# Kernel tuning notes

Hardware: AMD Instinct MI355X
Metric: run time of the kernel (lower is better)

## Reference

```python
import jax, jax.numpy as jnp
import numpy as np
from jax import lax

B, TENC, TMEL = 32, 512, 400
E, H, A, P, M, F, K = 512, 512, 512, 256, 128, 32, 31


def setup_inputs() -> dict:
    key = jax.random.key(0)
    ks = jax.random.split(key, 20)
    def rn(i, shape, fan_in):
        return jax.random.normal(ks[i], shape, jnp.float32) / np.float32(np.sqrt(fan_in))
    return dict(
        enc_outputs=jax.random.normal(ks[0], (B, TENC, 2 * E), jnp.float32),
        mel_spec_true=jax.random.normal(ks[1], (B, TMEL, M), jnp.float32),
        text_lens=jax.random.randint(ks[2], (B,), 0, TENC),
        mel_spec_lens=jax.random.randint(ks[3], (B,), 0, TMEL),
        max_text_len=TENC,
        pre_w1=rn(4, (M, P), M), pre_w2=rn(5, (P, P), P),
        attn_wi=rn(6, (P + E, 3 * H), P + E), attn_wh=rn(7, (H, 3 * H), H),
        attn_bi=jnp.zeros((3 * H,), jnp.float32), attn_bh=jnp.zeros((3 * H,), jnp.float32),
        q_w=rn(8, (H, A), H), k_w=rn(9, (2 * E, A), 2 * E),
        score_w=rn(10, (A, 1), A), score_b=jnp.zeros((1,), jnp.float32),
        loc_conv_w=rn(11, (F, 2, K), 2 * K), loc_w=rn(12, (F, A), F), loc_b=jnp.zeros((A,), jnp.float32),
        out_wi=rn(13, (A + H, 3 * H), A + H), out_wh=rn(14, (H, 3 * H), H),
        out_bi=jnp.zeros((3 * H,), jnp.float32), out_bh=jnp.zeros((3 * H,), jnp.float32),
        dec_w=rn(15, (H + A, M), H + A), dec_b=jnp.zeros((M,), jnp.float32),
        gate_w=rn(16, (H + A, 1), H + A), gate_b=jnp.zeros((1,), jnp.float32),
    )


def _gru_step(x, h, wi, wh, bi, bh):
    # single-step torch nn.GRU cell; gate order r, z, n
    gi = x @ wi + bi
    gh = h @ wh + bh
    ir, iz, inn = jnp.split(gi, 3, axis=-1)
    hr, hz, hn = jnp.split(gh, 3, axis=-1)
    r = jax.nn.sigmoid(ir + hr)
    z = jax.nn.sigmoid(iz + hz)
    n = jnp.tanh(inn + r * hn)
    return (1.0 - z) * n + z * h


def reference(enc_outputs, mel_spec_true, text_lens, mel_spec_lens, max_text_len,
              pre_w1, pre_w2, attn_wi, attn_wh, attn_bi, attn_bh,
              q_w, k_w, score_w, score_b, loc_conv_w, loc_w, loc_b,
              out_wi, out_wh, out_bi, out_bh, dec_w, dec_b, gate_w, gate_b):
    Bsz, Tenc, _ = enc_outputs.shape
    Tmel = mel_spec_true.shape[1]
    Hd = attn_wh.shape[0]
    Ad = k_w.shape[1]
    pad = (loc_conv_w.shape[2] - 1) // 2

    keys_p = enc_outputs @ k_w                                # [B,Tenc,A]
    enc_mask = jnp.arange(Tenc)[None, :] > text_lens[:, None]  # True = masked (t > len)

    def prenet(x):  # dropout disabled for determinism
        return jax.nn.relu(jax.nn.relu(x @ pre_w1) @ pre_w2)

    dec_in0 = prenet(jnp.zeros((Bsz, mel_spec_true.shape[2]), enc_outputs.dtype))
    carry0 = (jnp.zeros((Bsz, Hd), jnp.float32), jnp.zeros((Bsz, Hd), jnp.float32),
              jnp.zeros((Bsz, Tenc), jnp.float32), jnp.zeros((Bsz, Tenc), jnp.float32),
              jnp.zeros((Bsz, Ad), jnp.float32), dec_in0)

    def step(carry, _):
        h_attn, h_out, att_w, att_cum, ctx, dec_in = carry
        h_attn = _gru_step(jnp.concatenate([dec_in, ctx], -1), h_attn, attn_wi, attn_wh, attn_bi, attn_bh)
        loc_in = jnp.stack([att_w, att_cum], axis=1)           # [B,2,Tenc]
        loc = lax.conv_general_dilated(loc_in, loc_conv_w, (1,), [(pad, pad)],
                                       dimension_numbers=('NCH', 'OIH', 'NCH'))  # [B,F,Tenc]
        loc = jnp.swapaxes(loc, 1, 2) @ loc_w + loc_b          # [B,Tenc,A]
        q = (h_attn @ q_w)[:, None, :]                         # [B,1,A]
        s = (jnp.tanh(q + keys_p + loc) @ score_w + score_b)[..., 0]  # [B,Tenc]
        s = jnp.where(enc_mask, -jnp.inf, s)
        att_w = jax.nn.softmax(s, axis=1)
        ctx = jnp.einsum('bt,bta->ba', att_w, keys_p)
        att_cum = att_cum + att_w
        h_out = _gru_step(jnp.concatenate([h_attn, ctx], -1), h_out, out_wi, out_wh, out_bi, out_bh)
        att_h = jnp.concatenate([h_out, ctx], -1)
        mel = att_h @ dec_w + dec_b                            # [B,M]
        stop = (att_h @ gate_w + gate_b)[:, 0]                 # [B]
        dec_in = prenet(mel)                                   # teacher_force_ratio = 0
        return (h_attn, h_out, att_w, att_cum, ctx, dec_in), (mel, stop, att_w)

    _, (mels, gates, attns) = lax.scan(step, carry0, None, length=Tmel)
    mels = jnp.swapaxes(mels, 0, 1)    # [B,Tmel,M]
    gates = jnp.swapaxes(gates, 0, 1)  # [B,Tmel]
    attns = jnp.swapaxes(attns, 0, 1)  # [B,Tmel,Tenc]
    mel_mask = jnp.arange(Tmel)[None, :] > mel_spec_lens[:, None]
    masked_mel = jnp.where(mel_mask[:, :, None], 0.0, mels)
    masked_gate = jnp.where(mel_mask, 1000.0, gates)
    return masked_mel, masked_gate, attns, mel_mask
```

## Files before the change

kernel.cpp:

```cpp
#include <hip/hip_runtime.h>
#include <hip/hip_fp16.h>
#include <math.h>

#define NBLK 256
#define NTHR 1024

__device__ __forceinline__ float fast_rcp(float x) {
#if __has_builtin(__builtin_amdgcn_rcpf)
  return __builtin_amdgcn_rcpf(x);
#else
  return 1.f / x;
#endif
}
__device__ __forceinline__ float fast_sigmoid(float x) { return fast_rcp(1.f + __expf(-x)); }
__device__ __forceinline__ float fast_tanh(float x) { return 1.f - 2.f * fast_rcp(1.f + __expf(2.f * x)); }

union HU2 { unsigned int u; __half2 h; };
union HU4 { uint4 u; __half2 h[4]; };
__device__ __forceinline__ float2 cvt2(unsigned int u) { HU2 t; t.u = u; return __half22float2(t.h); }

__device__ __forceinline__ void sta(float* p, float v) {
  __hip_atomic_store(p, v, __ATOMIC_RELAXED, __HIP_MEMORY_SCOPE_AGENT);
}
__device__ __forceinline__ float lda(const float* p) {
  return __hip_atomic_load(p, __ATOMIC_RELAXED, __HIP_MEMORY_SCOPE_AGENT);
}

struct Params {
  const float *enc, *pre_w1, *pre_w2, *attn_bi, *attn_bh;
  const float *q_w, *k_w, *score_w, *score_b, *conv_w, *loc_w, *loc_b;
  const float *out_bi, *out_bh, *dec_b, *gate_b;
  const float *attn_wi, *attn_wh, *out_wi, *out_wh, *dec_w, *gate_w;
  const int *text_lens, *mel_lens;
  __half *hkeys, *gw1T, *gw2T, *decT, *pre1T, *pre2T, *gateh, *locwh, *qwT;
  float *hA, *hO, *attw, *attcum, *decin, *ebuf, *zpart, *ctxacc, *stateZ;
  int *done;
  unsigned *barc;
  float *out_mel, *out_gate, *out_attn, *out_mask;
};

__device__ __forceinline__ void gbar(unsigned* flags, unsigned* gen, unsigned e,
                                     int blk, int tid) {
  __syncthreads();
  if (tid == 0) {
    asm volatile("s_waitcnt vmcnt(0) lgkmcnt(0)" ::: "memory");
    __hip_atomic_store(&flags[blk], e, __ATOMIC_RELAXED, __HIP_MEMORY_SCOPE_AGENT);
  }
  if (blk == 0) {
    if (tid < 64) {
      while (true) {
        bool ok = true;
#pragma unroll
        for (int j = 0; j < 4; j++) {
          unsigned v = __hip_atomic_load(&flags[tid * 4 + j], __ATOMIC_RELAXED,
                                         __HIP_MEMORY_SCOPE_AGENT);
          ok &= (v >= e);
        }
        if (__all(ok)) break;
        __builtin_amdgcn_s_sleep(1);
      }
      if (tid == 0)
        __hip_atomic_store(gen, e, __ATOMIC_RELAXED, __HIP_MEMORY_SCOPE_AGENT);
    }
  } else {
    if (tid == 0) {
      while (__hip_atomic_load(gen, __ATOMIC_RELAXED, __HIP_MEMORY_SCOPE_AGENT) < e)
        __builtin_amdgcn_s_sleep(2);
    }
  }
  asm volatile("" ::: "memory");
  __syncthreads();
}

__global__ __launch_bounds__(512) void k_keys(Params p) {
  __shared__ float sA[16][132];
  __shared__ float sB[16][68];
  int tid = threadIdx.x;
  int row0 = blockIdx.x * 128, col0 = blockIdx.y * 64;
  float acc[4][4] = {};
  int r = tid >> 2, kq = tid & 3;
  int tx = tid & 15, ty = tid >> 4;
  for (int k0 = 0; k0 < 1024; k0 += 16) {
    __syncthreads();
    float4 a4 = *(const float4*)(p.enc + (size_t)(row0 + r) * 1024 + k0 + kq * 4);
    sA[kq * 4 + 0][r] = a4.x; sA[kq * 4 + 1][r] = a4.y;
    sA[kq * 4 + 2][r] = a4.z; sA[kq * 4 + 3][r] = a4.w;
    if (tid < 256) {
      int kb = tid >> 4, nb = (tid & 15) * 4;
      float4 b4 = *(const float4*)(p.k_w + (size_t)(k0 + kb) * 512 + col0 + nb);
      sB[kb][nb + 0] = b4.x; sB[kb][nb + 1] = b4.y;
      sB[kb][nb + 2] = b4.z; sB[kb][nb + 3] = b4.w;
    }
    __syncthreads();
#pragma unroll
    for (int k = 0; k < 16; k++) {
      float ar[4], br[4];
#pragma unroll
      for (int i = 0; i < 4; i++) { ar[i] = sA[k][ty * 4 + i]; br[i] = sB[k][tx * 4 + i]; }
#pragma unroll
      for (int i = 0; i < 4; i++)
#pragma unroll
        for (int j = 0; j < 4; j++) acc[i][j] = fmaf(ar[i], br[j], acc[i][j]);
    }
  }
#pragma unroll
  for (int i = 0; i < 4; i++)
#pragma unroll
    for (int j = 0; j < 4; j++)
      p.hkeys[(size_t)(row0 + ty * 4 + i) * 512 + col0 + tx * 4 + j] = __float2half(acc[i][j]);
}

__global__ __launch_bounds__(256) void k_repack(Params p) {
  const int gsz = gridDim.x * 256;
  const int t0 = blockIdx.x * 256 + threadIdx.x;
  for (int i = t0; i < 1280 * 512; i += gsz) {
    int r = i >> 9, u = i & 511;
    const float* src = (r < 768) ? p.attn_wi + (size_t)r * 1536 : p.attn_wh + (size_t)(r - 768) * 1536;
    __half2* d = (__half2*)(p.gw1T + ((size_t)i << 2));
    d[0] = __halves2half2(__float2half(src[u]), __float2half(src[512 + u]));
    d[1] = __halves2half2(__float2half(src[1024 + u]), __float2half(0.f));
  }
  for (int i = t0; i < 1536 * 512; i += gsz) {
    int r = i >> 9, u = i & 511;
    const float* src = (r < 1024) ? p.out_wi + (size_t)r * 1536 : p.out_wh + (size_t)(r - 1024) * 1536;
    __half2* d = (__half2*)(p.gw2T + ((size_t)i << 2));
    d[0] = __halves2half2(__float2half(src[u]), __float2half(src[512 + u]));
    d[1] = __halves2half2(__float2half(src[1024 + u]), __float2half(0.f));
  }
  for (int i = t0; i < 512 * 512; i += gsz) {
    int k = i >> 9, a = i & 511;
    p.qwT[(size_t)a * 512 + k] = __float2half(p.q_w[(size_t)k * 512 + a]);
  }
  for (int i = t0; i < 1024 * 128; i += gsz) {
    int k = i >> 7, m = i & 127;
    p.decT[(size_t)m * 1024 + k] = __float2half(p.dec_w[(size_t)k * 128 + m]);
  }
  for (int i = t0; i < 1024; i += gsz) p.gateh[i] = __float2half(p.gate_w[i]);
  for (int i = t0; i < 16384; i += gsz) p.locwh[i] = __float2half(p.loc_w[i]);
  for (int i = t0; i < 128 * 256; i += gsz) {
    int m = i >> 8, pc = i & 255;
    p.pre1T[(size_t)pc * 128 + m] = __float2half(p.pre_w1[(size_t)m * 256 + pc]);
  }
  for (int i = t0; i < 256 * 256; i += gsz) {
    int k = i >> 8, pc = i & 255;
    p.pre2T[(size_t)pc * 256 + k] = __float2half(p.pre_w2[(size_t)k * 256 + pc]);
  }
  for (int i = t0; i < 106496; i += gsz) p.stateZ[i] = 0.f;
  for (int i = t0; i < 16384; i += gsz) p.ctxacc[i] = 0.f;
  for (int i = t0; i < 512; i += gsz) p.barc[i] = 0u;
  for (int i = t0; i < 32; i += gsz) p.done[i] = 0;
  for (int i = t0; i < 12800; i += gsz) {
    int b = i / 400, t = i - b * 400;
    p.out_mask[i] = (t > p.mel_lens[b]) ? 1.f : 0.f;
  }
}

struct SMemMega {
  __half keysL[64 * 512];
  float ctxL[4][512];
  float invZ[4];
  union {
    struct { float x[4][1536]; float4 part4[16][64]; } gr;
    struct { float locS[64][33]; float aw[94]; float ac[94]; float hA_s[512]; float qS[512];
             float qpart[2][512]; float cpred[8][512]; float eS[64]; } s3;
    struct { float xh[1024]; float red[1024]; float mel[128]; float p1[256]; } s6;
  } u;
};

template <int DXI, int RPK>
__device__ __forceinline__ void gru_compute(SMemMega& sm, const uint2* w512,
    const float* __restrict__ bi, const float* __restrict__ bh,
    float* __restrict__ hnext, int ug, int b0, int tid) {
  const int u = tid & 15, b2 = (tid >> 4) & 3, ks = tid >> 6;
  const int uG = (ug << 4) + u;
  float ar = 0.f, az = 0.f, ani = 0.f, anh = 0.f;
  const uint2* w = w512 + (size_t)(ks * RPK) * 512 + uG;
#pragma unroll 8
  for (int j = 0; j < RPK; j++) {
    uint2 wv = w[(size_t)j * 512];
    int r = ks * RPK + j;
    float x = sm.u.gr.x[b2][r];
    float2 f0 = cvt2(wv.x);
    float2 f1 = cvt2(wv.y);
    ar = fmaf(x, f0.x, ar);
    az = fmaf(x, f0.y, az);
    float t = x * f1.x;
    if (r < DXI) ani += t; else anh += t;
  }
  sm.u.gr.part4[ks][(u << 2) + b2] = make_float4(ar, az, ani, anh);
  __syncthreads();
  if (tid < 64) {
    int uu = tid >> 2, bb2 = tid & 3;
    float4 s = make_float4(0.f, 0.f, 0.f, 0.f);
#pragma unroll
    for (int l = 0; l < 16; l++) {
      float4 v = sm.u.gr.part4[l][(uu << 2) + bb2];
      s.x += v.x; s.y += v.y; s.z += v.z; s.w += v.w;
    }
    int uGf = (ug << 4) + uu;
    float r = fast_sigmoid(s.x + bi[uGf] + bh[uGf]);
    float z = fast_sigmoid(s.y + bi[512 + uGf] + bh[512 + uGf]);
    float n = fast_tanh(s.z + bi[1024 + uGf] + r * (s.w + bh[1024 + uGf]));
    float hv = sm.u.gr.x[bb2][DXI + uGf];
    sta(&hnext[((size_t)(b0 + bb2) << 9) + uGf], (1.f - z) * n + z * hv);
  }
}

__global__ __launch_bounds__(NTHR) void mega(Params p) {
  __shared__ SMemMega sm;
  const int blk = blockIdx.x, tid = threadIdx.x;
  const int ug = blk & 31, bg = blk >> 5, b0 = bg * 4;
  const int bS = blk & 31, t8 = blk >> 5, t0g = t8 << 6;
  unsigned epoch = 0;
  unsigned* flags = p.barc;
  unsigned* gen = p.barc + 384;

  {
    const uint4* src = (const uint4*)(p.hkeys + (((size_t)(bS << 9) + t0g) << 9));
    uint4* dst = (uint4*)sm.keysL;
    for (int i = tid; i < 4096; i += NTHR) dst[i] = src[i];
    for (int i = tid; i < 2048; i += NTHR) sm.ctxL[i >> 9][i & 511] = 0.f;
  }
  __syncthreads();

#pragma clang loop unroll(disable)
  for (int step = 0; step < 400; step++) {
    const int par = step & 1;
    float* hA_prev = p.hA + par * 16384;
    float* hA_next = p.hA + (par ^ 1) * 16384;
    float* hO_prev = p.hO + par * 16384;
    float* hO_next = p.hO + (par ^ 1) * 16384;

    {
      if (ug == 0) {
        for (int i = tid; i < 2048; i += NTHR)
          sta(&p.ctxacc[(b0 << 9) + i], 0.f);
      }
      for (int i = tid; i < 1024; i += NTHR) {
        int b2 = i >> 8, r = i & 255;
        sm.u.gr.x[b2][r] = lda(&p.decin[((b0 + b2) << 8) + r]);
      }
      for (int i = tid; i < 2048; i += NTHR) {
        int b2 = i >> 9, a = i & 511;
        sm.u.gr.x[b2][256 + a] = sm.ctxL[b2][a];
      }
      for (int i = tid; i < 2048; i += NTHR) {
        int b2 = i >> 9, a = i & 511;
        sm.u.gr.x[b2][768 + a] = lda(&hA_prev[((b0 + b2) << 9) + a]);
      }
      __syncthreads();
      gru_compute<768, 80>(sm, (const uint2*)p.gw1T, p.attn_bi, p.attn_bh,
                           hA_next, ug, b0, tid);
    }
    gbar(flags, gen, ++epoch, blk, tid);

    {
      const int tlen = p.text_lens[bS];
      for (int j = tid; j < 94; j += NTHR) {
        int pp = t0g - 15 + j;
        bool ok = (unsigned)pp < 512u;
        sm.u.s3.aw[j] = ok ? lda(&p.attw[(bS << 9) + pp]) : 0.f;
        sm.u.s3.ac[j] = ok ? lda(&p.attcum[(bS << 9) + pp]) : 0.f;
      }
      if (tid < 512) sm.u.s3.hA_s[tid] = lda(&hA_next[(bS << 9) + tid]);
      __syncthreads();
      for (int i = tid; i < 2048; i += NTHR) {
        int tt = i >> 5, f = i & 31;
        const float* w0 = p.conv_w + f * 62;
        float a = 0.f;
#pragma unroll
        for (int k = 0; k < 31; k++)
          a = fmaf(w0[k], sm.u.s3.aw[tt + k], fmaf(w0[31 + k], sm.u.s3.ac[tt + k], a));
        sm.u.s3.locS[tt][f] = a;
      }
      {
        int a = tid & 511, ks = tid >> 9;
        const HU4* qp = (const HU4*)(p.qwT + (size_t)a * 512 + ks * 256);
        float q0 = 0.f, q1 = 0.f;
#pragma unroll 4
        for (int it = 0; it < 32; it++) {
          HU4 raw = qp[it];
          int kb = ks * 256 + it * 8;
#pragma unroll
          for (int h2 = 0; h2 < 4; h2++) {
            float2 w = __half22float2(raw.h[h2]);
            q0 = fmaf(sm.u.s3.hA_s[kb + h2 * 2], w.x, q0);
            q1 = fmaf(sm.u.s3.hA_s[kb + h2 * 2 + 1], w.y, q1);
          }
        }
        sm.u.s3.qpart[ks][a] = q0 + q1;
      }
      __syncthreads();
      if (tid < 512)
        sm.u.s3.qS[tid] = sm.u.s3.qpart[0][tid] + sm.u.s3.qpart[1][tid] + p.loc_b[tid];
      __syncthreads();
      const int lane = tid & 63, wv = tid >> 6;
      float acc[4][8];
      float4 qA = *(const float4*)&sm.u.s3.qS[lane * 8];
      float4 qB = *(const float4*)&sm.u.s3.qS[lane * 8 + 4];
#pragma unroll
      for (int j = 0; j < 4; j++) {
        int tL = wv * 4 + j;
        HU4 raw; raw.u = *(const uint4*)&sm.keysL[tL * 512 + lane * 8];
        float2 k0 = __half22float2(raw.h[0]), k1 = __half22float2(raw.h[1]);
        float2 k2 = __half22float2(raw.h[2]), k3 = __half22float2(raw.h[3]);
        acc[j][0] = qA.x + k0.x; acc[j][1] = qA.y + k0.y;
        acc[j][2] = qA.z + k1.x; acc[j][3] = qA.w + k1.y;
        acc[j][4] = qB.x + k2.x; acc[j][5] = qB.y + k2.y;
        acc[j][6] = qB.z + k3.x; acc[j][7] = qB.w + k3.y;
      }
#pragma unroll 4
      for (int f = 0; f < 32; f++) {
        HU4 rw; rw.u = *(const uint4*)(p.locwh + (size_t)f * 512 + lane * 8);
        float2 w0 = __half22float2(rw.h[0]), w1 = __half22float2(rw.h[1]);
        float2 w2 = __half22float2(rw.h[2]), w3 = __half22float2(rw.h[3]);
#pragma unroll
        for (int j = 0; j < 4; j++) {
          float lf = sm.u.s3.locS[wv * 4 + j][f];
          acc[j][0] = fmaf(lf, w0.x, acc[j][0]); acc[j][1] = fmaf(lf, w0.y, acc[j][1]);
          acc[j][2] = fmaf(lf, w1.x, acc[j][2]); acc[j][3] = fmaf(lf, w1.y, acc[j][3]);
          acc[j][4] = fmaf(lf, w2.x, acc[j][4]); acc[j][5] = fmaf(lf, w2.y, acc[j][5]);
          acc[j][6] = fmaf(lf, w3.x, acc[j][6]); acc[j][7] = fmaf(lf, w3.y, acc[j][7]);
        }
      }
      float4 sA = *(const float4*)(p.score_w + lane * 8);
      float4 sB = *(const float4*)(p.score_w + lane * 8 + 4);
      float sbias = p.score_b[0];
      float e_reg[4];
#pragma unroll
      for (int j = 0; j < 4; j++) {
        float pv = fast_tanh(acc[j][0]) * sA.x + fast_tanh(acc[j][1]) * sA.y +
                   fast_tanh(acc[j][2]) * sA.z + fast_tanh(acc[j][3]) * sA.w +
                   fast_tanh(acc[j][4]) * sB.x + fast_tanh(acc[j][5]) * sB.y +
                   fast_tanh(acc[j][6]) * sB.z + fast_tanh(acc[j][7]) * sB.w;
#pragma unroll
        for (int off = 32; off > 0; off >>= 1) pv += __shfl_xor(pv, off, 64);
        int t = t0g + wv * 4 + j;
        e_reg[j] = (t > tlen) ? 0.f : __expf(pv + sbias);
      }
      if (lane == 0) {
#pragma unroll
        for (int j = 0; j < 4; j++) sm.u.s3.eS[wv * 4 + j] = e_reg[j];
      }
      float cp[8] = {0.f, 0.f, 0.f, 0.f, 0.f, 0.f, 0.f, 0.f};
#pragma unroll
      for (int j = 0; j < 4; j++) {
        int tL = wv * 4 + j;
        HU4 raw; raw.u = *(const uint4*)&sm.keysL[tL * 512 + lane * 8];
        float2 k0 = __half22float2(raw.h[0]), k1 = __half22float2(raw.h[1]);
        float2 k2 = __half22float2(raw.h[2]), k3 = __half22float2(raw.h[3]);
        float e = e_reg[j];
        cp[0] = fmaf(e, k0.x, cp[0]); cp[1] = fmaf(e, k0.y, cp[1]);
        cp[2] = fmaf(e, k1.x, cp[2]); cp[3] = fmaf(e, k1.y, cp[3]);
        cp[4] = fmaf(e, k2.x, cp[4]); cp[5] = fmaf(e, k2.y, cp[5]);
        cp[6] = fmaf(e, k3.x, cp[6]); cp[7] = fmaf(e, k3.y, cp[7]);
      }
      __syncthreads();
      if (wv < 8) {
        float4* r0 = (float4*)&sm.u.s3.cpred[wv][lane * 8];
        r0[0] = make_float4(cp[0], cp[1], cp[2], cp[3]);
        r0[1] = make_float4(cp[4], cp[5], cp[6], cp[7]);
      }
      __syncthreads();
      if (wv >= 8) {
        float* r0 = &sm.u.s3.cpred[wv - 8][lane * 8];
#pragma unroll
        for (int i = 0; i < 8; i++) r0[i] += cp[i];
      }
      __syncthreads();
      if (tid < 512) {
        float s = 0.f;
#pragma unroll
        for (int j = 0; j < 8; j++) s += sm.u.s3.cpred[j][tid];
        atomicAdd(&p.ctxacc[(bS << 9) + tid], s);
      }
      if (tid < 64) {
        float e = sm.u.s3.eS[tid];
        sta(&p.ebuf[(bS << 9) + t0g + tid], e);
        float z = e;
#pragma unroll
        for (int off = 32; off > 0; off >>= 1) z += __shfl_xor(z, off, 64);
        if (tid == 0) sta(&p.zpart[bS * 8 + t8], z);
      }
    }
    gbar(flags, gen, ++epoch, blk, tid);

    {
      if (tid < 4) {
        float Z = 0.f;
#pragma unroll
        for (int j = 0; j < 8; j++) Z += lda(&p.zpart[(b0 + tid) * 8 + j]);
        sm.invZ[tid] = fast_rcp(Z);
      }
      __syncthreads();
      for (int i = tid; i < 2048; i += NTHR) {
        int b2 = i >> 9, a = i & 511;
        sm.ctxL[b2][a] = lda(&p.ctxacc[((b0 + b2) << 9) + a]) * sm.invZ[b2];
      }
      if (ug == 0) {
        for (int i = tid; i < 2048; i += NTHR) {
          int b2 = i >> 9, t = i & 511;
          int bb = b0 + b2;
          float v = lda(&p.ebuf[(bb << 9) + t]) * sm.invZ[b2];
          sta(&p.attw[(bb << 9) + t], v);
          float oc = lda(&p.attcum[(bb << 9) + t]);
          sta(&p.attcum[(bb << 9) + t], oc + v);
          p.out_attn[(size_t)bb * 204800 + (size_t)step * 512 + t] = v;
        }
      }
      __syncthreads();
      for (int i = tid; i < 2048; i += NTHR) {
        int b2 = i >> 9, a = i & 511;
        sm.u.gr.x[b2][a] = lda(&hA_next[((b0 + b2) << 9) + a]);
      }
      for (int i = tid; i < 2048; i += NTHR) {
        int b2 = i >> 9, a = i & 511;
        sm.u.gr.x[b2][512 + a] = sm.ctxL[b2][a];
      }
      for (int i = tid; i < 2048; i += NTHR) {
        int b2 = i >> 9, a = i & 511;
        sm.u.gr.x[b2][1024 + a] = lda(&hO_prev[((b0 + b2) << 9) + a]);
      }
      __syncthreads();
      gru_compute<1024, 96>(sm, (const uint2*)p.gw2T, p.out_bi, p.out_bh,
                            hO_next, ug, b0, tid);
      asm volatile("s_waitcnt vmcnt(0)" ::: "memory");
      __syncthreads();
      if (tid < 4) atomicAdd(&p.done[b0 + tid], 1);
      if (ug < 4) {
        const int bb = b0 + ug;
        if (tid == 0) {
          int target = 32 * (step + 1);
          while (__hip_atomic_load(&p.done[bb], __ATOMIC_RELAXED,
                                   __HIP_MEMORY_SCOPE_AGENT) < target)
            __builtin_amdgcn_s_sleep(2);
        }
        __syncthreads();
        sm.u.s6.xh[tid] = (tid < 512) ? lda(&hO_next[(bb << 9) + tid])
                                      : sm.ctxL[ug][tid - 512];
        __syncthreads();
        bool masked = step > p.mel_lens[bb];
        {
          int m = tid & 127, ks = tid >> 7;
          const HU4* dp = (const HU4*)(p.decT + (size_t)m * 1024 + ks * 128);
          float a = 0.f;
#pragma unroll 4
          for (int it = 0; it < 16; it++) {
            HU4 raw = dp[it];
            int kb = ks * 128 + it * 8;
#pragma unroll
            for (int h2 = 0; h2 < 4; h2++) {
              float2 w = __half22float2(raw.h[h2]);
              a = fmaf(sm.u.s6.xh[kb + h2 * 2], w.x, a);
              a = fmaf(sm.u.s6.xh[kb + h2 * 2 + 1], w.y, a);
            }
          }
          sm.u.s6.red[tid] = a;
        }
        __syncthreads();
        if (tid < 128) {
          float mv = p.dec_b[tid];
#pragma unroll
          for (int j = 0; j < 8; j++) mv += sm.u.s6.red[tid + j * 128];
          sm.u.s6.mel[tid] = mv;
          p.out_mel[(size_t)bb * 51200 + (size_t)step * 128 + tid] = masked ? 0.f : mv;
        }
        __syncthreads();
        sm.u.s6.red[tid] = sm.u.s6.xh[tid] * __half2float(p.gateh[tid]);
        __syncthreads();
        if (tid < 64) {
          float g = 0.f;
#pragma unroll
          for (int j = 0; j < 16; j++) g += sm.u.s6.red[tid + j * 64];
#pragma unroll
          for (int off = 32; off > 0; off >>= 1) g += __shfl_xor(g, off, 64);
          if (tid == 0) p.out_gate[bb * 400 + step] = masked ? 1000.f : (g + p.gate_b[0]);
        }
        __syncthreads();
        {
          int pc = tid & 255, ks = tid >> 8;
          const HU4* wp = (const HU4*)(p.pre1T + (size_t)pc * 128 + ks * 32);
          float a = 0.f;
#pragma unroll
          for (int it = 0; it < 4; it++) {
            HU4 raw = wp[it];
            int kb = ks * 32 + it * 8;
#pragma unroll
            for (int h2 = 0; h2 < 4; h2++) {
              float2 w = __half22float2(raw.h[h2]);
              a = fmaf(sm.u.s6.mel[kb + h2 * 2], w.x, a);
              a = fmaf(sm.u.s6.mel[kb + h2 * 2 + 1], w.y, a);
            }
          }
          sm.u.s6.red[tid] = a;
        }
        __syncthreads();
        if (tid < 256) {
          float a = sm.u.s6.red[tid] + sm.u.s6.red[tid + 256] +
                    sm.u.s6.red[tid + 512] + sm.u.s6.red[tid + 768];
          sm.u.s6.p1[tid] = fmaxf(a, 0.f);
        }
        __syncthreads();
        {
          int pc = tid & 255, ks = tid >> 8;
          const HU4* wp = (const HU4*)(p.pre2T + (size_t)pc * 256 + ks * 64);
          float a = 0.f;
#pragma unroll
          for (int it = 0; it < 8; it++) {
            HU4 raw = wp[it];
            int kb = ks * 64 + it * 8;
#pragma unroll
            for (int h2 = 0; h2 < 4; h2++) {
              float2 w = __half22float2(raw.h[h2]);
              a = fmaf(sm.u.s6.p1[kb + h2 * 2], w.x, a);
              a = fmaf(sm.u.s6.p1[kb + h2 * 2 + 1], w.y, a);
            }
          }
          sm.u.s6.red[tid] = a;
        }
        __syncthreads();
        if (tid < 256) {
          float a = sm.u.s6.red[tid] + sm.u.s6.red[tid + 256] +
                    sm.u.s6.red[tid + 512] + sm.u.s6.red[tid + 768];
          sta(&p.decin[(bb << 8) + tid], fmaxf(a, 0.f));
        }
      }
    }
    gbar(flags, gen, ++epoch, blk, tid);
  }
}

extern "C" void kernel_launch(void* const* d_in, const int* in_sizes, int n_in,
                              void* d_out, int out_size, void* d_ws, size_t ws_size,
                              hipStream_t stream) {
  Params p;
  p.enc       = (const float*)d_in[0];
  p.text_lens = (const int*)d_in[2];
  p.mel_lens  = (const int*)d_in[3];
  p.pre_w1    = (const float*)d_in[5];
  p.pre_w2    = (const float*)d_in[6];
  p.attn_wi   = (const float*)d_in[7];
  p.attn_wh   = (const float*)d_in[8];
  p.attn_bi   = (const float*)d_in[9];
  p.attn_bh   = (const float*)d_in[10];
  p.q_w       = (const float*)d_in[11];
  p.k_w       = (const float*)d_in[12];
  p.score_w   = (const float*)d_in[13];
  p.score_b   = (const float*)d_in[14];
  p.conv_w    = (const float*)d_in[15];
  p.loc_w     = (const float*)d_in[16];
  p.loc_b     = (const float*)d_in[17];
  p.out_wi    = (const float*)d_in[18];
  p.out_wh    = (const float*)d_in[19];
  p.out_bi    = (const float*)d_in[20];
  p.out_bh    = (const float*)d_in[21];
  p.dec_w     = (const float*)d_in[22];
  p.dec_b     = (const float*)d_in[23];
  p.gate_w    = (const float*)d_in[24];
  p.gate_b    = (const float*)d_in[25];

  float* ws = (float*)d_ws;
  p.hkeys  = (__half*)(ws);
  p.gw1T   = (__half*)(ws + 4194304);
  p.gw2T   = (__half*)(ws + 5505024);
  p.decT   = (__half*)(ws + 7077888);
  p.pre1T  = (__half*)(ws + 7143424);
  p.pre2T  = (__half*)(ws + 7159808);
  p.gateh  = (__half*)(ws + 7192576);
  p.locwh  = (__half*)(ws + 7193088);
  p.qwT    = (__half*)(ws + 7201280);
  p.hA     = ws + 7332352;
  p.hO     = ws + 7365120;
  p.attw   = ws + 7397888;
  p.attcum = ws + 7414272;
  p.decin  = ws + 7430656;
  p.stateZ = p.hA;
  p.ebuf   = ws + 7438848;
  p.zpart  = ws + 7455232;
  p.ctxacc = ws + 7455488;
  p.done   = (int*)(ws + 7471872);
  p.barc   = (unsigned*)(ws + 7471904);
  float* out = (float*)d_out;
  p.out_mel  = out;
  p.out_gate = out + 1638400;
  p.out_attn = out + 1651200;
  p.out_mask = out + 8204800;

  k_repack<<<2048, 256, 0, stream>>>(p);
  k_keys<<<dim3(128, 8), 512, 0, stream>>>(p);
  void* args[] = { (void*)&p };
  hipLaunchCooperativeKernel((const void*)mega, dim3(NBLK), dim3(NTHR), args, 0, stream);
}
```

Baseline: 41.97 ms.

## Replace global barriers with per-group flag sync and redundantly compute decoder/prenet per block

Removes the three grid-wide centralized barriers per step and replaces them with per-batch-group and per-attention-slice flag arrays, so blocks only wait on the producers they actually depend on. The mel/gate projection and prenet, previously done by only four blocks after an extra counter wait, are now recomputed redundantly in every block at the start of the next step (with an extra trailing step to emit the last outputs). ctxacc is double-buffered by parity so its zeroing does not race with accumulation. This trades extra redundant matvec work and more flag polling for shorter critical-path synchronization.

```diff
diff --git a/kernel.cpp b/kernel.cpp
--- a/kernel.cpp
+++ b/kernel.cpp
@@ -25,51 +25,27 @@
 __device__ __forceinline__ float lda(const float* p) {
   return __hip_atomic_load(p, __ATOMIC_RELAXED, __HIP_MEMORY_SCOPE_AGENT);
 }
+__device__ __forceinline__ int ldai(const int* p) {
+  return __hip_atomic_load(p, __ATOMIC_RELAXED, __HIP_MEMORY_SCOPE_AGENT);
+}
 
 struct Params {
   const float *enc, *pre_w1, *pre_w2, *attn_bi, *attn_bh;
   const float *q_w, *k_w, *score_w, *score_b, *conv_w, *loc_w, *loc_b;
-  const float *out_bi, *out_bh, *dec_b, *gate_b;
-  const float *attn_wi, *attn_wh, *out_wi, *out_wh, *dec_w, *gate_w;
+  const float *out_bi, *out_bh, *dec_b, *gate_b, *gate_w;
+  const float *attn_wi, *attn_wh, *out_wi, *out_wh, *dec_w;
   const int *text_lens, *mel_lens;
-  __half *hkeys, *gw1T, *gw2T, *decT, *pre1T, *pre2T, *gateh, *locwh, *qwT;
-  float *hA, *hO, *attw, *attcum, *decin, *ebuf, *zpart, *ctxacc, *stateZ;
-  int *done;
-  unsigned *barc;
+  __half *hkeys, *gw1T, *gw2T, *decT, *pre1T, *pre2T, *locwh, *qwT;
+  float *hA, *hO, *attw, *attcum, *ebuf, *zpart, *ctxacc, *stateZ;
+  int *flagsA, *flagsB, *flagsC;
   float *out_mel, *out_gate, *out_attn, *out_mask;
 };
 
-__device__ __forceinline__ void gbar(unsigned* flags, unsigned* gen, unsigned e,
-                                     int blk, int tid) {
-  __syncthreads();
+__device__ __forceinline__ void set_flag(int* f, int v, int tid) {
   if (tid == 0) {
     asm volatile("s_waitcnt vmcnt(0) lgkmcnt(0)" ::: "memory");
-    __hip_atomic_store(&flags[blk], e, __ATOMIC_RELAXED, __HIP_MEMORY_SCOPE_AGENT);
-  }
-  if (blk == 0) {
-    if (tid < 64) {
-      while (true) {
-        bool ok = true;
-#pragma unroll
-        for (int j = 0; j < 4; j++) {
-          unsigned v = __hip_atomic_load(&flags[tid * 4 + j], __ATOMIC_RELAXED,
-                                         __HIP_MEMORY_SCOPE_AGENT);
-          ok &= (v >= e);
-        }
-        if (__all(ok)) break;
-        __builtin_amdgcn_s_sleep(1);
-      }
-      if (tid == 0)
-        __hip_atomic_store(gen, e, __ATOMIC_RELAXED, __HIP_MEMORY_SCOPE_AGENT);
-    }
-  } else {
-    if (tid == 0) {
-      while (__hip_atomic_load(gen, __ATOMIC_RELAXED, __HIP_MEMORY_SCOPE_AGENT) < e)
-        __builtin_amdgcn_s_sleep(2);
-    }
-  }
-  asm volatile("" ::: "memory");
-  __syncthreads();
+    __hip_atomic_store(f, v, __ATOMIC_RELAXED, __HIP_MEMORY_SCOPE_AGENT);
+  }
 }
 
 __global__ __launch_bounds__(512) void k_keys(Params p) {
@@ -135,7 +111,6 @@
     int k = i >> 7, m = i & 127;
     p.decT[(size_t)m * 1024 + k] = __float2half(p.dec_w[(size_t)k * 128 + m]);
   }
-  for (int i = t0; i < 1024; i += gsz) p.gateh[i] = __float2half(p.gate_w[i]);
   for (int i = t0; i < 16384; i += gsz) p.locwh[i] = __float2half(p.loc_w[i]);
   for (int i = t0; i < 128 * 256; i += gsz) {
     int m = i >> 8, pc = i & 255;
@@ -145,10 +120,9 @@
     int k = i >> 8, pc = i & 255;
     p.pre2T[(size_t)pc * 256 + k] = __float2half(p.pre_w2[(size_t)k * 256 + pc]);
   }
-  for (int i = t0; i < 106496; i += gsz) p.stateZ[i] = 0.f;
-  for (int i = t0; i < 16384; i += gsz) p.ctxacc[i] = 0.f;
-  for (int i = t0; i < 512; i += gsz) p.barc[i] = 0u;
-  for (int i = t0; i < 32; i += gsz) p.done[i] = 0;
+  for (int i = t0; i < 98304; i += gsz) p.stateZ[i] = 0.f;
+  for (int i = t0; i < 32768; i += gsz) p.ctxacc[i] = 0.f;
+  for (int i = t0; i < 768; i += gsz) p.flagsA[i] = 0;
   for (int i = t0; i < 12800; i += gsz) {
     int b = i / 400, t = i - b * 400;
     p.out_mask[i] = (t > p.mel_lens[b]) ? 1.f : 0.f;
@@ -160,10 +134,10 @@
   float ctxL[4][512];
   float invZ[4];
   union {
-    struct { float x[4][1536]; float4 part4[16][64]; } gr;
+    struct { float x[4][1536]; float4 part4[16][64];
+             float xh[4][1024]; float red[1024]; float mel4[4][128]; float p1b[4][256]; } gr;
     struct { float locS[64][33]; float aw[94]; float ac[94]; float hA_s[512]; float qS[512];
              float qpart[2][512]; float cpred[8][512]; float eS[64]; } s3;
-    struct { float xh[1024]; float red[1024]; float mel[128]; float p1[256]; } s6;
   } u;
 };
 
@@ -211,9 +185,6 @@
   const int blk = blockIdx.x, tid = threadIdx.x;
   const int ug = blk & 31, bg = blk >> 5, b0 = bg * 4;
   const int bS = blk & 31, t8 = blk >> 5, t0g = t8 << 6;
-  unsigned epoch = 0;
-  unsigned* flags = p.barc;
-  unsigned* gen = p.barc + 384;
 
   {
     const uint4* src = (const uint4*)(p.hkeys + (((size_t)(bS << 9) + t0g) << 9));
@@ -224,36 +195,139 @@
   __syncthreads();
 
 #pragma clang loop unroll(disable)
-  for (int step = 0; step < 400; step++) {
+  for (int step = 0; step <= 400; step++) {
     const int par = step & 1;
     float* hA_prev = p.hA + par * 16384;
     float* hA_next = p.hA + (par ^ 1) * 16384;
     float* hO_prev = p.hO + par * 16384;
     float* hO_next = p.hO + (par ^ 1) * 16384;
 
-    {
-      if (ug == 0) {
-        for (int i = tid; i < 2048; i += NTHR)
-          sta(&p.ctxacc[(b0 << 9) + i], 0.f);
-      }
-      for (int i = tid; i < 1024; i += NTHR) {
-        int b2 = i >> 8, r = i & 255;
-        sm.u.gr.x[b2][r] = lda(&p.decin[((b0 + b2) << 8) + r]);
-      }
+    if (tid < 64) {
+      const int* f = p.flagsC + (bg << 5);
+      while (true) {
+        int v = (tid < 32) ? ldai(&f[tid]) : 0x7fffffff;
+        if (__all(v >= step)) break;
+        __builtin_amdgcn_s_sleep(1);
+      }
+    }
+    __syncthreads();
+    if (ug == 0) {
+      for (int i = tid; i < 2048; i += NTHR)
+        sta(&p.ctxacc[((par ^ 1) << 14) + (b0 << 9) + i], 0.f);
+    }
+    for (int i = tid; i < 4096; i += NTHR) {
+      int b2 = i >> 10, r = i & 1023;
+      sm.u.gr.xh[b2][r] = (r < 512) ? lda(&hO_prev[((size_t)(b0 + b2) << 9) + r])
+                                    : sm.ctxL[b2][r - 512];
+    }
+    if (step < 400) {
       for (int i = tid; i < 2048; i += NTHR) {
         int b2 = i >> 9, a = i & 511;
         sm.u.gr.x[b2][256 + a] = sm.ctxL[b2][a];
       }
       for (int i = tid; i < 2048; i += NTHR) {
         int b2 = i >> 9, a = i & 511;
-        sm.u.gr.x[b2][768 + a] = lda(&hA_prev[((b0 + b2) << 9) + a]);
-      }
-      __syncthreads();
-      gru_compute<768, 80>(sm, (const uint2*)p.gw1T, p.attn_bi, p.attn_bh,
-                           hA_next, ug, b0, tid);
-    }
-    gbar(flags, gen, ++epoch, blk, tid);
-
+        sm.u.gr.x[b2][768 + a] = lda(&hA_prev[((size_t)(b0 + b2) << 9) + a]);
+      }
+    }
+    __syncthreads();
+    {
+      int m = tid & 127, b2 = (tid >> 7) & 3, ks = tid >> 9;
+      const HU4* dp = (const HU4*)(p.decT + (size_t)m * 1024 + ks * 512);
+      float a = 0.f;
+#pragma unroll 4
+      for (int it = 0; it < 64; it++) {
+        HU4 raw = dp[it];
+        int kb = ks * 512 + it * 8;
+#pragma unroll
+        for (int h2 = 0; h2 < 4; h2++) {
+          float2 w = __half22float2(raw.h[h2]);
+          a = fmaf(sm.u.gr.xh[b2][kb + h2 * 2], w.x, a);
+          a = fmaf(sm.u.gr.xh[b2][kb + h2 * 2 + 1], w.y, a);
+        }
+      }
+      sm.u.gr.red[tid] = a;
+    }
+    __syncthreads();
+    if (tid < 512) {
+      int m = tid & 127, b2 = tid >> 7;
+      float mv = sm.u.gr.red[tid] + sm.u.gr.red[tid + 512] + p.dec_b[m];
+      sm.u.gr.mel4[b2][m] = mv;
+      if (ug == 0 && step >= 1) {
+        int bb = b0 + b2;
+        bool masked = (step - 1) > p.mel_lens[bb];
+        p.out_mel[(size_t)bb * 51200 + (size_t)(step - 1) * 128 + m] = masked ? 0.f : mv;
+      }
+    }
+    if (ug == 0 && step >= 1 && tid < 256) {
+      int b2 = tid >> 6, lane = tid & 63;
+      float g = 0.f;
+#pragma unroll
+      for (int j = 0; j < 16; j++) {
+        int k = lane + (j << 6);
+        g = fmaf(sm.u.gr.xh[b2][k], p.gate_w[k], g);
+      }
+#pragma unroll
+      for (int off = 32; off > 0; off >>= 1) g += __shfl_xor(g, off, 64);
+      if (lane == 0) {
+        int bb = b0 + b2;
+        bool masked = (step - 1) > p.mel_lens[bb];
+        p.out_gate[bb * 400 + (step - 1)] = masked ? 1000.f : (g + p.gate_b[0]);
+      }
+    }
+    if (step == 400) return;
+    __syncthreads();
+    {
+      int pc = tid & 255, b2 = tid >> 8;
+      const HU4* wp = (const HU4*)(p.pre1T + (size_t)pc * 128);
+      float a = 0.f;
+#pragma unroll 4
+      for (int it = 0; it < 16; it++) {
+        HU4 raw = wp[it];
+        int kb = it * 8;
+#pragma unroll
+        for (int h2 = 0; h2 < 4; h2++) {
+          float2 w = __half22float2(raw.h[h2]);
+          a = fmaf(sm.u.gr.mel4[b2][kb + h2 * 2], w.x, a);
+          a = fmaf(sm.u.gr.mel4[b2][kb + h2 * 2 + 1], w.y, a);
+        }
+      }
+      __syncthreads();
+      sm.u.gr.p1b[b2][pc] = fmaxf(a, 0.f);
+    }
+    __syncthreads();
+    {
+      int pc = tid & 255, b2 = tid >> 8;
+      const HU4* wp = (const HU4*)(p.pre2T + (size_t)pc * 256);
+      float a = 0.f;
+#pragma unroll 4
+      for (int it = 0; it < 32; it++) {
+        HU4 raw = wp[it];
+        int kb = it * 8;
+#pragma unroll
+        for (int h2 = 0; h2 < 4; h2++) {
+          float2 w = __half22float2(raw.h[h2]);
+          a = fmaf(sm.u.gr.p1b[b2][kb + h2 * 2], w.x, a);
+          a = fmaf(sm.u.gr.p1b[b2][kb + h2 * 2 + 1], w.y, a);
+        }
+      }
+      sm.u.gr.x[b2][pc] = (step == 0) ? 0.f : fmaxf(a, 0.f);
+    }
+    __syncthreads();
+    gru_compute<768, 80>(sm, (const uint2*)p.gw1T, p.attn_bi, p.attn_bh,
+                         hA_next, ug, b0, tid);
+    __syncthreads();
+    set_flag(&p.flagsA[blk], step + 1, tid);
+
+    if (tid < 64) {
+      const int* f = p.flagsA + ((bS >> 2) << 5);
+      while (true) {
+        int v = (tid < 32) ? ldai(&f[tid]) : 0x7fffffff;
+        if (__all(v >= step + 1)) break;
+        __builtin_amdgcn_s_sleep(1);
+      }
+    }
+    __syncthreads();
     {
       const int tlen = p.text_lens[bS];
       for (int j = tid; j < 94; j += NTHR) {
@@ -372,7 +446,7 @@
         float s = 0.f;
 #pragma unroll
         for (int j = 0; j < 8; j++) s += sm.u.s3.cpred[j][tid];
-        atomicAdd(&p.ctxacc[(bS << 9) + tid], s);
+        atomicAdd(&p.ctxacc[(par << 14) + (bS << 9) + tid], s);
       }
       if (tid < 64) {
         float e = sm.u.s3.eS[tid];
@@ -383,8 +457,21 @@
         if (tid == 0) sta(&p.zpart[bS * 8 + t8], z);
       }
     }
-    gbar(flags, gen, ++epoch, blk, tid);
-
+    __syncthreads();
+    set_flag(&p.flagsB[blk], step + 1, tid);
+
+    if (tid < 64) {
+      while (true) {
+        int v = 0x7fffffff;
+        if (tid < 32) {
+          int tt8 = tid >> 2, b = b0 + (tid & 3);
+          v = ldai(&p.flagsB[(tt8 << 5) + b]);
+        }
+        if (__all(v >= step + 1)) break;
+        __builtin_amdgcn_s_sleep(1);
+      }
+    }
+    __syncthreads();
     {
       if (tid < 4) {
         float Z = 0.f;
@@ -395,7 +482,7 @@
       __syncthreads();
       for (int i = tid; i < 2048; i += NTHR) {
         int b2 = i >> 9, a = i & 511;
-        sm.ctxL[b2][a] = lda(&p.ctxacc[((b0 + b2) << 9) + a]) * sm.invZ[b2];
+        sm.ctxL[b2][a] = lda(&p.ctxacc[(par << 14) + ((b0 + b2) << 9) + a]) * sm.invZ[b2];
       }
       if (ug == 0) {
         for (int i = tid; i < 2048; i += NTHR) {
@@ -408,125 +495,25 @@
           p.out_attn[(size_t)bb * 204800 + (size_t)step * 512 + t] = v;
         }
       }
-      __syncthreads();
       for (int i = tid; i < 2048; i += NTHR) {
         int b2 = i >> 9, a = i & 511;
-        sm.u.gr.x[b2][a] = lda(&hA_next[((b0 + b2) << 9) + a]);
-      }
+        sm.u.gr.x[b2][a] = lda(&hA_next[((size_t)(b0 + b2) << 9) + a]);
+      }
+      __syncthreads();
       for (int i = tid; i < 2048; i += NTHR) {
         int b2 = i >> 9, a = i & 511;
         sm.u.gr.x[b2][512 + a] = sm.ctxL[b2][a];
       }
       for (int i = tid; i < 2048; i += NTHR) {
         int b2 = i >> 9, a = i & 511;
-        sm.u.gr.x[b2][1024 + a] = lda(&hO_prev[((b0 + b2) << 9) + a]);
+        sm.u.gr.x[b2][1024 + a] = lda(&hO_prev[((size_t)(b0 + b2) << 9) + a]);
       }
       __syncthreads();
       gru_compute<1024, 96>(sm, (const uint2*)p.gw2T, p.out_bi, p.out_bh,
                             hO_next, ug, b0, tid);
-      asm volatile("s_waitcnt vmcnt(0)" ::: "memory");
-      __syncthreads();
-      if (tid < 4) atomicAdd(&p.done[b0 + tid], 1);
-      if (ug < 4) {
-        const int bb = b0 + ug;
-        if (tid == 0) {
-          int target = 32 * (step + 1);
-          while (__hip_atomic_load(&p.done[bb], __ATOMIC_RELAXED,
-                                   __HIP_MEMORY_SCOPE_AGENT) < target)
-            __builtin_amdgcn_s_sleep(2);
-        }
-        __syncthreads();
-        sm.u.s6.xh[tid] = (tid < 512) ? lda(&hO_next[(bb << 9) + tid])
-                                      : sm.ctxL[ug][tid - 512];
-        __syncthreads();
-        bool masked = step > p.mel_lens[bb];
-        {
-          int m = tid & 127, ks = tid >> 7;
-          const HU4* dp = (const HU4*)(p.decT + (size_t)m * 1024 + ks * 128);
-          float a = 0.f;
-#pragma unroll 4
-          for (int it = 0; it < 16; it++) {
-            HU4 raw = dp[it];
-            int kb = ks * 128 + it * 8;
-#pragma unroll
-            for (int h2 = 0; h2 < 4; h2++) {
-              float2 w = __half22float2(raw.h[h2]);
-              a = fmaf(sm.u.s6.xh[kb + h2 * 2], w.x, a);
-              a = fmaf(sm.u.s6.xh[kb + h2 * 2 + 1], w.y, a);
-            }
-          }
-          sm.u.s6.red[tid] = a;
-        }
-        __syncthreads();
-        if (tid < 128) {
-          float mv = p.dec_b[tid];
-#pragma unroll
-          for (int j = 0; j < 8; j++) mv += sm.u.s6.red[tid + j * 128];
-          sm.u.s6.mel[tid] = mv;
-          p.out_mel[(size_t)bb * 51200 + (size_t)step * 128 + tid] = masked ? 0.f : mv;
-        }
-        __syncthreads();
-        sm.u.s6.red[tid] = sm.u.s6.xh[tid] * __half2float(p.gateh[tid]);
-        __syncthreads();
-        if (tid < 64) {
-          float g = 0.f;
-#pragma unroll
-          for (int j = 0; j < 16; j++) g += sm.u.s6.red[tid + j * 64];
-#pragma unroll
-          for (int off = 32; off > 0; off >>= 1) g += __shfl_xor(g, off, 64);
-          if (tid == 0) p.out_gate[bb * 400 + step] = masked ? 1000.f : (g + p.gate_b[0]);
-        }
-        __syncthreads();
-        {
-          int pc = tid & 255, ks = tid >> 8;
-          const HU4* wp = (const HU4*)(p.pre1T + (size_t)pc * 128 + ks * 32);
-          float a = 0.f;
-#pragma unroll
-          for (int it = 0; it < 4; it++) {
-            HU4 raw = wp[it];
-            int kb = ks * 32 + it * 8;
-#pragma unroll
-            for (int h2 = 0; h2 < 4; h2++) {
-              float2 w = __half22float2(raw.h[h2]);
-              a = fmaf(sm.u.s6.mel[kb + h2 * 2], w.x, a);
-              a = fmaf(sm.u.s6.mel[kb + h2 * 2 + 1], w.y, a);
-            }
-          }
-          sm.u.s6.red[tid] = a;
-        }
-        __syncthreads();
-        if (tid < 256) {
-          float a = sm.u.s6.red[tid] + sm.u.s6.red[tid + 256] +
-                    sm.u.s6.red[tid + 512] + sm.u.s6.red[tid + 768];
-          sm.u.s6.p1[tid] = fmaxf(a, 0.f);
-        }
-        __syncthreads();
-        {
-          int pc = tid & 255, ks = tid >> 8;
-          const HU4* wp = (const HU4*)(p.pre2T + (size_t)pc * 256 + ks * 64);
-          float a = 0.f;
-#pragma unroll
-          for (int it = 0; it < 8; it++) {
-            HU4 raw = wp[it];
-            int kb = ks * 64 + it * 8;
-#pragma unroll
-            for (int h2 = 0; h2 < 4; h2++) {
-              float2 w = __half22float2(raw.h[h2]);
-              a = fmaf(sm.u.s6.p1[kb + h2 * 2], w.x, a);
-              a = fmaf(sm.u.s6.p1[kb + h2 * 2 + 1], w.y, a);
-            }
-          }
-          sm.u.s6.red[tid] = a;
-        }
-        __syncthreads();
-        if (tid < 256) {
-          float a = sm.u.s6.red[tid] + sm.u.s6.red[tid + 256] +
-                    sm.u.s6.red[tid + 512] + sm.u.s6.red[tid + 768];
-          sta(&p.decin[(bb << 8) + tid], fmaxf(a, 0.f));
-        }
-      }
-    }
-    gbar(flags, gen, ++epoch, blk, tid);
+    }
+    __syncthreads();
+    set_flag(&p.flagsC[blk], step + 1, tid);
   }
 }
 
@@ -566,20 +553,19 @@
   p.decT   = (__half*)(ws + 7077888);
   p.pre1T  = (__half*)(ws + 7143424);
   p.pre2T  = (__half*)(ws + 7159808);
-  p.gateh  = (__half*)(ws + 7192576);
-  p.locwh  = (__half*)(ws + 7193088);
-  p.qwT    = (__half*)(ws + 7201280);
-  p.hA     = ws + 7332352;
-  p.hO     = ws + 7365120;
-  p.attw   = ws + 7397888;
-  p.attcum = ws + 7414272;
-  p.decin  = ws + 7430656;
+  p.locwh  = (__half*)(ws + 7192576);
+  p.qwT    = (__half*)(ws + 7200768);
+  p.hA     = ws + 7331840;
+  p.hO     = ws + 7364608;
+  p.attw   = ws + 7397376;
+  p.attcum = ws + 7413760;
   p.stateZ = p.hA;
-  p.ebuf   = ws + 7438848;
-  p.zpart  = ws + 7455232;
-  p.ctxacc = ws + 7455488;
-  p.done   = (int*)(ws + 7471872);
-  p.barc   = (unsigned*)(ws + 7471904);
+  p.ebuf   = ws + 7430144;
+  p.zpart  = ws + 7446528;
+  p.ctxacc = ws + 7446784;
+  p.flagsA = (int*)(ws + 7479552);
+  p.flagsB = p.flagsA + 256;
+  p.flagsC = p.flagsA + 512;
   float* out = (float*)d_out;
   p.out_mel  = out;
   p.out_gate = out + 1638400;
```

Result: slower. 61.53 ms (+46.6%).

## Move decoder/prenet stage to next step start and replace grid barrier with targeted flags

Applied to the files above, without the earlier changes.

Moves the mel/gate projection and prenet of step t to the start of step t+1, running on the four blocks per batch group. This lets the tail wait on a per-batch done counter be dropped. The first global barrier after the attention GRU becomes point-to-point flags. Each block waits only for the decin of its own batch group, and the attention-stage block waits only for the 32 GRU blocks that produce its batch. The aim is shorter serialized critical paths and fewer full-grid syncs per step, at the cost of an extra loop iteration and more intricate flag ordering that could race.

```diff
diff --git a/kernel.cpp b/kernel.cpp
--- a/kernel.cpp
+++ b/kernel.cpp
@@ -23,6 +23,9 @@
   __hip_atomic_store(p, v, __ATOMIC_RELAXED, __HIP_MEMORY_SCOPE_AGENT);
 }
 __device__ __forceinline__ float lda(const float* p) {
+  return __hip_atomic_load(p, __ATOMIC_RELAXED, __HIP_MEMORY_SCOPE_AGENT);
+}
+__device__ __forceinline__ int ldai(const int* p) {
   return __hip_atomic_load(p, __ATOMIC_RELAXED, __HIP_MEMORY_SCOPE_AGENT);
 }
 
@@ -34,7 +37,7 @@
   const int *text_lens, *mel_lens;
   __half *hkeys, *gw1T, *gw2T, *decT, *pre1T, *pre2T, *gateh, *locwh, *qwT;
   float *hA, *hO, *attw, *attcum, *decin, *ebuf, *zpart, *ctxacc, *stateZ;
-  int *done;
+  int *flagsA, *flagsD;
   unsigned *barc;
   float *out_mel, *out_gate, *out_attn, *out_mask;
 };
@@ -147,8 +150,8 @@
   }
   for (int i = t0; i < 106496; i += gsz) p.stateZ[i] = 0.f;
   for (int i = t0; i < 16384; i += gsz) p.ctxacc[i] = 0.f;
+  for (int i = t0; i < 288; i += gsz) p.flagsA[i] = 0;
   for (int i = t0; i < 512; i += gsz) p.barc[i] = 0u;
-  for (int i = t0; i < 32; i += gsz) p.done[i] = 0;
   for (int i = t0; i < 12800; i += gsz) {
     int b = i / 400, t = i - b * 400;
     p.out_mask[i] = (t > p.mel_lens[b]) ? 1.f : 0.f;
@@ -224,36 +227,161 @@
   __syncthreads();
 
 #pragma clang loop unroll(disable)
-  for (int step = 0; step < 400; step++) {
+  for (int step = 0; step <= 400; step++) {
     const int par = step & 1;
     float* hA_prev = p.hA + par * 16384;
     float* hA_next = p.hA + (par ^ 1) * 16384;
     float* hO_prev = p.hO + par * 16384;
     float* hO_next = p.hO + (par ^ 1) * 16384;
 
-    {
-      if (ug == 0) {
-        for (int i = tid; i < 2048; i += NTHR)
-          sta(&p.ctxacc[(b0 << 9) + i], 0.f);
-      }
-      for (int i = tid; i < 1024; i += NTHR) {
-        int b2 = i >> 8, r = i & 255;
-        sm.u.gr.x[b2][r] = lda(&p.decin[((b0 + b2) << 8) + r]);
-      }
-      for (int i = tid; i < 2048; i += NTHR) {
-        int b2 = i >> 9, a = i & 511;
-        sm.u.gr.x[b2][256 + a] = sm.ctxL[b2][a];
-      }
-      for (int i = tid; i < 2048; i += NTHR) {
-        int b2 = i >> 9, a = i & 511;
-        sm.u.gr.x[b2][768 + a] = lda(&hA_prev[((b0 + b2) << 9) + a]);
-      }
-      __syncthreads();
-      gru_compute<768, 80>(sm, (const uint2*)p.gw1T, p.attn_bi, p.attn_bh,
-                           hA_next, ug, b0, tid);
-    }
-    gbar(flags, gen, ++epoch, blk, tid);
-
+    if (ug == 0) {
+      for (int i = tid; i < 2048; i += NTHR)
+        sta(&p.ctxacc[(b0 << 9) + i], 0.f);
+    }
+    if (ug < 4) {
+      const int bb = b0 + ug;
+      sm.u.s6.xh[tid] = (tid < 512) ? lda(&hO_prev[(bb << 9) + tid])
+                                    : sm.ctxL[ug][tid - 512];
+      __syncthreads();
+      const int prev = step - 1;
+      bool masked = prev > p.mel_lens[bb];
+      {
+        int m = tid & 127, ks = tid >> 7;
+        const HU4* dp = (const HU4*)(p.decT + (size_t)m * 1024 + ks * 128);
+        float a = 0.f;
+#pragma unroll 4
+        for (int it = 0; it < 16; it++) {
+          HU4 raw = dp[it];
+          int kb = ks * 128 + it * 8;
+#pragma unroll
+          for (int h2 = 0; h2 < 4; h2++) {
+            float2 w = __half22float2(raw.h[h2]);
+            a = fmaf(sm.u.s6.xh[kb + h2 * 2], w.x, a);
+            a = fmaf(sm.u.s6.xh[kb + h2 * 2 + 1], w.y, a);
+          }
+        }
+        sm.u.s6.red[tid] = a;
+      }
+      __syncthreads();
+      if (tid < 128) {
+        float mv = p.dec_b[tid];
+#pragma unroll
+        for (int j = 0; j < 8; j++) mv += sm.u.s6.red[tid + j * 128];
+        sm.u.s6.mel[tid] = mv;
+        if (step >= 1)
+          p.out_mel[(size_t)bb * 51200 + (size_t)prev * 128 + tid] = masked ? 0.f : mv;
+      }
+      __syncthreads();
+      sm.u.s6.red[tid] = sm.u.s6.xh[tid] * __half2float(p.gateh[tid]);
+      __syncthreads();
+      if (tid < 64) {
+        float g = 0.f;
+#pragma unroll
+        for (int j = 0; j < 16; j++) g += sm.u.s6.red[tid + j * 64];
+#pragma unroll
+        for (int off = 32; off > 0; off >>= 1) g += __shfl_xor(g, off, 64);
+        if (tid == 0 && step >= 1)
+          p.out_gate[bb * 400 + prev] = masked ? 1000.f : (g + p.gate_b[0]);
+      }
+      __syncthreads();
+      if (step < 400) {
+        {
+          int pc = tid & 255, ks = tid >> 8;
+          const HU4* wp = (const HU4*)(p.pre1T + (size_t)pc * 128 + ks * 32);
+          float a = 0.f;
+#pragma unroll
+          for (int it = 0; it < 4; it++) {
+            HU4 raw = wp[it];
+            int kb = ks * 32 + it * 8;
+#pragma unroll
+            for (int h2 = 0; h2 < 4; h2++) {
+              float2 w = __half22float2(raw.h[h2]);
+              a = fmaf(sm.u.s6.mel[kb + h2 * 2], w.x, a);
+              a = fmaf(sm.u.s6.mel[kb + h2 * 2 + 1], w.y, a);
+            }
+          }
+          sm.u.s6.red[tid] = a;
+        }
+        __syncthreads();
+        if (tid < 256) {
+          float a = sm.u.s6.red[tid] + sm.u.s6.red[tid + 256] +
+                    sm.u.s6.red[tid + 512] + sm.u.s6.red[tid + 768];
+          sm.u.s6.p1[tid] = fmaxf(a, 0.f);
+        }
+        __syncthreads();
+        {
+          int pc = tid & 255, ks = tid >> 8;
+          const HU4* wp = (const HU4*)(p.pre2T + (size_t)pc * 256 + ks * 64);
+          float a = 0.f;
+#pragma unroll
+          for (int it = 0; it < 8; it++) {
+            HU4 raw = wp[it];
+            int kb = ks * 64 + it * 8;
+#pragma unroll
+            for (int h2 = 0; h2 < 4; h2++) {
+              float2 w = __half22float2(raw.h[h2]);
+              a = fmaf(sm.u.s6.p1[kb + h2 * 2], w.x, a);
+              a = fmaf(sm.u.s6.p1[kb + h2 * 2 + 1], w.y, a);
+            }
+          }
+          sm.u.s6.red[tid] = a;
+        }
+        __syncthreads();
+        if (tid < 256) {
+          float a = sm.u.s6.red[tid] + sm.u.s6.red[tid + 256] +
+                    sm.u.s6.red[tid + 512] + sm.u.s6.red[tid + 768];
+          sta(&p.decin[(bb << 8) + tid], (step == 0) ? 0.f : fmaxf(a, 0.f));
+        }
+        __syncthreads();
+        set_flagD: ;
+        if (tid == 0) {
+          asm volatile("s_waitcnt vmcnt(0) lgkmcnt(0)" ::: "memory");
+          __hip_atomic_store(&p.flagsD[(bg << 2) + ug], step + 1, __ATOMIC_RELAXED,
+                             __HIP_MEMORY_SCOPE_AGENT);
+        }
+      }
+    }
+    if (step == 400) return;
+    __syncthreads();
+    for (int i = tid; i < 2048; i += NTHR) {
+      int b2 = i >> 9, a = i & 511;
+      sm.u.gr.x[b2][256 + a] = sm.ctxL[b2][a];
+    }
+    for (int i = tid; i < 2048; i += NTHR) {
+      int b2 = i >> 9, a = i & 511;
+      sm.u.gr.x[b2][768 + a] = lda(&hA_prev[((size_t)(b0 + b2) << 9) + a]);
+    }
+    if (tid < 64) {
+      while (true) {
+        int v = (tid < 4) ? ldai(&p.flagsD[(bg << 2) + tid]) : 0x7fffffff;
+        if (__all(v >= step + 1)) break;
+        __builtin_amdgcn_s_sleep(1);
+      }
+    }
+    __syncthreads();
+    for (int i = tid; i < 1024; i += NTHR) {
+      int b2 = i >> 8, r = i & 255;
+      sm.u.gr.x[b2][r] = lda(&p.decin[((b0 + b2) << 8) + r]);
+    }
+    __syncthreads();
+    gru_compute<768, 80>(sm, (const uint2*)p.gw1T, p.attn_bi, p.attn_bh,
+                         hA_next, ug, b0, tid);
+    __syncthreads();
+    if (tid == 0) {
+      asm volatile("s_waitcnt vmcnt(0) lgkmcnt(0)" ::: "memory");
+      __hip_atomic_store(&p.flagsA[blk], step + 1, __ATOMIC_RELAXED,
+                         __HIP_MEMORY_SCOPE_AGENT);
+    }
+
+    if (tid < 64) {
+      const int* f = p.flagsA + ((bS >> 2) << 5);
+      while (true) {
+        int v = (tid < 32) ? ldai(&f[tid]) : 0x7fffffff;
+        if (__all(v >= step + 1)) break;
+        __builtin_amdgcn_s_sleep(1);
+      }
+    }
+    __syncthreads();
     {
       const int tlen = p.text_lens[bS];
       for (int j = tid; j < 94; j += NTHR) {
@@ -411,7 +539,7 @@
       __syncthreads();
       for (int i = tid; i < 2048; i += NTHR) {
         int b2 = i >> 9, a = i & 511;
-        sm.u.gr.x[b2][a] = lda(&hA_next[((b0 + b2) << 9) + a]);
+        sm.u.gr.x[b2][a] = lda(&hA_next[((size_t)(b0 + b2) << 9) + a]);
       }
       for (int i = tid; i < 2048; i += NTHR) {
         int b2 = i >> 9, a = i & 511;
@@ -419,112 +547,11 @@
       }
       for (int i = tid; i < 2048; i += NTHR) {
         int b2 = i >> 9, a = i & 511;
-        sm.u.gr.x[b2][1024 + a] = lda(&hO_prev[((b0 + b2) << 9) + a]);
+        sm.u.gr.x[b2][1024 + a] = lda(&hO_prev[((size_t)(b0 + b2) << 9) + a]);
       }
       __syncthreads();
       gru_compute<1024, 96>(sm, (const uint2*)p.gw2T, p.out_bi, p.out_bh,
                             hO_next, ug, b0, tid);
-      asm volatile("s_waitcnt vmcnt(0)" ::: "memory");
-      __syncthreads();
-      if (tid < 4) atomicAdd(&p.done[b0 + tid], 1);
-      if (ug < 4) {
-        const int bb = b0 + ug;
-        if (tid == 0) {
-          int target = 32 * (step + 1);
-          while (__hip_atomic_load(&p.done[bb], __ATOMIC_RELAXED,
-                                   __HIP_MEMORY_SCOPE_AGENT) < target)
-            __builtin_amdgcn_s_sleep(2);
-        }
-        __syncthreads();
-        sm.u.s6.xh[tid] = (tid < 512) ? lda(&hO_next[(bb << 9) + tid])
-                                      : sm.ctxL[ug][tid - 512];
-        __syncthreads();
-        bool masked = step > p.mel_lens[bb];
-        {
-          int m = tid & 127, ks = tid >> 7;
-          const HU4* dp = (const HU4*)(p.decT + (size_t)m * 1024 + ks * 128);
-          float a = 0.f;
-#pragma unroll 4
-          for (int it = 0; it < 16; it++) {
-            HU4 raw = dp[it];
-            int kb = ks * 128 + it * 8;
-#pragma unroll
-            for (int h2 = 0; h2 < 4; h2++) {
-              float2 w = __half22float2(raw.h[h2]);
-              a = fmaf(sm.u.s6.xh[kb + h2 * 2], w.x, a);
-              a = fmaf(sm.u.s6.xh[kb + h2 * 2 + 1], w.y, a);
-            }
-          }
-          sm.u.s6.red[tid] = a;
-        }
-        __syncthreads();
-        if (tid < 128) {
-          float mv = p.dec_b[tid];
-#pragma unroll
-          for (int j = 0; j < 8; j++) mv += sm.u.s6.red[tid + j * 128];
-          sm.u.s6.mel[tid] = mv;
-          p.out_mel[(size_t)bb * 51200 + (size_t)step * 128 + tid] = masked ? 0.f : mv;
-        }
-        __syncthreads();
-        sm.u.s6.red[tid] = sm.u.s6.xh[tid] * __half2float(p.gateh[tid]);
-        __syncthreads();
-        if (tid < 64) {
-          float g = 0.f;
-#pragma unroll
-          for (int j = 0; j < 16; j++) g += sm.u.s6.red[tid + j * 64];
-#pragma unroll
-          for (int off = 32; off > 0; off >>= 1) g += __shfl_xor(g, off, 64);
-          if (tid == 0) p.out_gate[bb * 400 + step] = masked ? 1000.f : (g + p.gate_b[0]);
-        }
-        __syncthreads();
-        {
-          int pc = tid & 255, ks = tid >> 8;
-          const HU4* wp = (const HU4*)(p.pre1T + (size_t)pc * 128 + ks * 32);
-          float a = 0.f;
-#pragma unroll
-          for (int it = 0; it < 4; it++) {
-            HU4 raw = wp[it];
-            int kb = ks * 32 + it * 8;
-#pragma unroll
-            for (int h2 = 0; h2 < 4; h2++) {
-              float2 w = __half22float2(raw.h[h2]);
-              a = fmaf(sm.u.s6.mel[kb + h2 * 2], w.x, a);
-              a = fmaf(sm.u.s6.mel[kb + h2 * 2 + 1], w.y, a);
-            }
-          }
-          sm.u.s6.red[tid] = a;
-        }
-        __syncthreads();
-        if (tid < 256) {
-          float a = sm.u.s6.red[tid] + sm.u.s6.red[tid + 256] +
-                    sm.u.s6.red[tid + 512] + sm.u.s6.red[tid + 768];
-          sm.u.s6.p1[tid] = fmaxf(a, 0.f);
-        }
-        __syncthreads();
-        {
-          int pc = tid & 255, ks = tid >> 8;
-          const HU4* wp = (const HU4*)(p.pre2T + (size_t)pc * 256 + ks * 64);
-          float a = 0.f;
-#pragma unroll
-          for (int it = 0; it < 8; it++) {
-            HU4 raw = wp[it];
-            int kb = ks * 64 + it * 8;
-#pragma unroll
-            for (int h2 = 0; h2 < 4; h2++) {
-              float2 w = __half22float2(raw.h[h2]);
-              a = fmaf(sm.u.s6.p1[kb + h2 * 2], w.x, a);
-              a = fmaf(sm.u.s6.p1[kb + h2 * 2 + 1], w.y, a);
-            }
-          }
-          sm.u.s6.red[tid] = a;
-        }
-        __syncthreads();
-        if (tid < 256) {
-          float a = sm.u.s6.red[tid] + sm.u.s6.red[tid + 256] +
-                    sm.u.s6.red[tid + 512] + sm.u.s6.red[tid + 768];
-          sta(&p.decin[(bb << 8) + tid], fmaxf(a, 0.f));
-        }
-      }
     }
     gbar(flags, gen, ++epoch, blk, tid);
   }
@@ -578,8 +605,9 @@
   p.ebuf   = ws + 7438848;
   p.zpart  = ws + 7455232;
   p.ctxacc = ws + 7455488;
-  p.done   = (int*)(ws + 7471872);
-  p.barc   = (unsigned*)(ws + 7471904);
+  p.flagsA = (int*)(ws + 7471872);
+  p.flagsD = p.flagsA + 256;
+  p.barc   = (unsigned*)(ws + 7472160);
   float* out = (float*)d_out;
   p.out_mel  = out;
   p.out_gate = out + 1638400;
```

Result: no change. 42.52 ms (+1.3%).
